# Kernel tuning notes

Hardware: AMD Instinct MI355X
Metric: run time of the kernel (lower is better)

Reference implementation:

```python
import jax, jax.numpy as jnp
import numpy as np

B = 524288
H = 20          # heads
NUM_EX = 13     # embedding rows
EMB = 3         # embedding dim
FEAT_IN, FEAT_OUT = 3, 5
HEAD_IN, HEAD_HID = 8, 10


def setup_inputs() -> dict:
    key = jax.random.key(0)
    ks = jax.random.split(key, 12)
    e = jax.random.randint(ks[0], (B, H), 0, NUM_EX)
    f = jax.random.normal(ks[1], (B, H * FEAT_IN), dtype=jnp.float32)
    # embedding table; row 0 zeroed as in the torch __init__
    emb = jax.random.normal(ks[2], (NUM_EX, EMB), dtype=jnp.float32) * 0.1
    emb = emb.at[0].set(0.0)
    # features Linear(3 -> 5), stored as (in, out) so y = x @ Wf + bf
    Wf = jax.random.normal(ks[3], (FEAT_IN, FEAT_OUT), dtype=jnp.float32) * 0.5
    bf = jax.random.normal(ks[4], (FEAT_OUT,), dtype=jnp.float32) * 0.1
    # 20 parallel head MLPs, batched over the head axis
    W1 = jax.random.normal(ks[5], (H, HEAD_IN, HEAD_HID), dtype=jnp.float32) * 0.3
    b1 = jax.random.normal(ks[6], (H, HEAD_HID), dtype=jnp.float32) * 0.1
    W2 = jax.random.normal(ks[7], (H, HEAD_HID), dtype=jnp.float32) * 0.3
    b2 = jax.random.normal(ks[8], (H,), dtype=jnp.float32) * 0.1
    # output Linear(20 -> 1)
    Wo = jax.random.normal(ks[9], (H, 1), dtype=jnp.float32) * 0.3
    bo = jax.random.normal(ks[10], (1,), dtype=jnp.float32) * 0.1
    return {"e": e, "f": f, "emb": emb, "Wf": Wf, "bf": bf,
            "W1": W1, "b1": b1, "W2": W2, "b2": b2, "Wo": Wo, "bo": bo}


def reference(e, f, emb, Wf, bf, W1, b1, W2, b2, Wo, bo):
    ev = emb[e]                                    # (B, 20, 3) embedding lookup
    fv = f.reshape(-1, H, FEAT_IN) @ Wf + bf       # (B, 20, 5)
    x = jnp.concatenate([ev, fv], axis=2)          # (B, 20, 8)
    # all 20 heads as one batched matmul instead of a Python loop
    h1 = jax.nn.leaky_relu(jnp.einsum('bhi,hio->bho', x, W1) + b1)  # (B, 20, 10)
    h = jax.nn.softplus(jnp.einsum('bho,ho->bh', h1, W2) + b2)      # (B, 20)
    return h @ Wo + bo                             # (B, 1)
```

## Files before the change

kernel.cpp:

```cpp
#include <hip/hip_runtime.h>


#define HH   20
#define NEX  13
#define TST  12
#define WS_M 0
#define WS_T 640
#define NT   512

typedef __attribute__((ext_vector_type(4))) _Float16 half4;

__device__ __forceinline__ float softplus_fast(float x) {
    return fmaxf(x, 0.0f) + __logf(1.0f + __expf(-fabsf(x)));
}

__global__ void airfit_setup(const float* __restrict__ emb,
                             const float* __restrict__ Wf,
                             const float* __restrict__ bf,
                             const float* __restrict__ W1,
                             const float* __restrict__ b1,
                             float* __restrict__ ws)
{
    int t = blockIdx.x * 256 + threadIdx.x;
    if (t < HH * 3 * 10) {
        int h = t / 30, c = (t / 10) % 3, o = t % 10;
        float a = 0.0f;
        for (int q = 0; q < 5; ++q)
            a += Wf[c * 5 + q] * W1[(h * 8 + 3 + q) * 10 + o];
        ws[WS_M + (h * 3 + c) * 10 + o] = a;
    }
    if (t < HH * NEX * 10) {
        int h = t / (NEX * 10), idx = (t / 10) % NEX, o = t % 10;
        float a = b1[h * 10 + o];
        for (int i = 0; i < 3; ++i)
            a += emb[idx * 3 + i] * W1[(h * 8 + i) * 10 + o];
        for (int q = 0; q < 5; ++q)
            a += bf[q] * W1[(h * 8 + 3 + q) * 10 + o];
        ws[WS_T + (h * NEX + idx) * TST + o] = a;
    }
}

__global__ __launch_bounds__(NT, 4) void airfit_kernel(
    const int*   __restrict__ e,   const float* __restrict__ f,
    const float* __restrict__ ws,  const float* __restrict__ W2,
    const float* __restrict__ b2,  const float* __restrict__ Wo,
    const float* __restrict__ bo,  float* __restrict__ out, int B)
{
    __shared__ half4          s_fh[15][NT];
    __shared__ unsigned short s_e[NT * 6];
    __shared__ float          s_T[HH * NEX * TST];

    const int tid  = threadIdx.x;
    const int base = blockIdx.x * NT;
    const int nIt  = min(NT, B - base);

    for (int t = tid; t < HH * NEX * TST; t += NT)
        s_T[t] = ws[WS_T + t];

    {
        const float4* fg = reinterpret_cast<const float4*>(f) + (size_t)base * 15;
        const int total4 = nIt * 15;
#pragma unroll
        for (int k = 0; k < 15; ++k) {
            int idx = tid + NT * k;
            if (idx < total4) {
                float4 v = fg[idx];
                int item = idx / 15, c4 = idx - item * 15;
                half4 hv = { (_Float16)v.x, (_Float16)v.y,
                             (_Float16)v.z, (_Float16)v.w };
                s_fh[c4][item] = hv;
            }
        }
    }

    {
        const int4* eg = reinterpret_cast<const int4*>(e) + (size_t)base * 5;
        const int total4 = nIt * 5;
#pragma unroll
        for (int k = 0; k < 5; ++k) {
            int idx = tid + NT * k;
            if (idx < total4) {
                int4 iv = eg[idx];
                int item = idx / 5, g = idx - item * 5;
                unsigned p = (unsigned)iv.x | ((unsigned)iv.y << 4) |
                             ((unsigned)iv.z << 8) | ((unsigned)iv.w << 12);
                s_e[item * 6 + g] = (unsigned short)p;
            }
        }
    }

    __syncthreads();

    if (tid >= nIt) return;
    const float* M = ws + WS_M;

    const unsigned* e32 = reinterpret_cast<const unsigned*>(s_e);
    unsigned ew[3] = { e32[tid * 3 + 0], e32[tid * 3 + 1], e32[tid * 3 + 2] };

    float acc = bo[0];

#pragma unroll
    for (int g = 0; g < 5; ++g) {
        half4 a0 = s_fh[3 * g + 0][tid];
        half4 a1 = s_fh[3 * g + 1][tid];
        half4 a2 = s_fh[3 * g + 2][tid];
        float ff[12] = { (float)a0.x, (float)a0.y, (float)a0.z, (float)a0.w,
                         (float)a1.x, (float)a1.y, (float)a1.z, (float)a1.w,
                         (float)a2.x, (float)a2.y, (float)a2.z, (float)a2.w };
        unsigned gw  = ew[g >> 1] >> ((g & 1) * 16);

#pragma unroll
        for (int t = 0; t < 4; ++t) {
            const int h = 4 * g + t;
            int idx = (gw >> (4 * t)) & 0xf;

            const float* Trow = s_T + (h * NEX + idx) * TST;
            float4 t0 = *reinterpret_cast<const float4*>(Trow);
            float4 t1 = *reinterpret_cast<const float4*>(Trow + 4);
            float2 t2 = *reinterpret_cast<const float2*>(Trow + 8);
            float pre[10] = { t0.x, t0.y, t0.z, t0.w,
                              t1.x, t1.y, t1.z, t1.w, t2.x, t2.y };

            float g0 = ff[3 * t + 0], g1 = ff[3 * t + 1], g2 = ff[3 * t + 2];
            float hacc = b2[h];
#pragma unroll
            for (int o = 0; o < 10; ++o) {
                float a = pre[o];
                a = fmaf(g0, M[(h * 3 + 0) * 10 + o], a);
                a = fmaf(g1, M[(h * 3 + 1) * 10 + o], a);
                a = fmaf(g2, M[(h * 3 + 2) * 10 + o], a);
                a = fmaxf(a, 0.01f * a);
                hacc = fmaf(a, W2[h * 10 + o], hacc);
            }
            acc = fmaf(softplus_fast(hacc), Wo[h], acc);
        }
    }

    out[base + tid] = acc;
}

extern "C" void kernel_launch(void* const* d_in, const int* in_sizes, int n_in,
                              void* d_out, int out_size, void* d_ws, size_t ws_size,
                              hipStream_t stream) {
    const int*   e   = (const int*)  d_in[0];
    const float* f   = (const float*)d_in[1];
    const float* emb = (const float*)d_in[2];
    const float* Wf  = (const float*)d_in[3];
    const float* bf  = (const float*)d_in[4];
    const float* W1  = (const float*)d_in[5];
    const float* b1  = (const float*)d_in[6];
    const float* W2  = (const float*)d_in[7];
    const float* b2  = (const float*)d_in[8];
    const float* Wo  = (const float*)d_in[9];
    const float* bo  = (const float*)d_in[10];
    float* out = (float*)d_out;
    float* ws  = (float*)d_ws;

    int B = in_sizes[0] / HH;

    airfit_setup<<<11, 256, 0, stream>>>(emb, Wf, bf, W1, b1, ws);

    int blocks = (B + NT - 1) / NT;
    airfit_kernel<<<blocks, NT, 0, stream>>>(e, f, ws, W2, b2, Wo, bo, out, B);
}
```

Baseline: 253.4 us.

## Switch head MLP to packed fp16 math and drop shared-memory input staging

Precomputed tables and weights are now stored as packed fp16 pairs. The hidden layer uses packed half FMAs plus fdot2 for the W2 reduction, which is meant to cut ALU instruction count. Inputs e and f are read directly per thread instead of being staged through LDS, which shrinks shared memory use and allows occupancy to rise to 8 blocks per CU. The trade-off is that per-thread strided global loads are less coalesced, and doing the pre-activation in fp16 lowers accuracy.

Result: slower. 279.9 us (+10.4%).

```diff
diff --git a/kernel.cpp b/kernel.cpp
--- a/kernel.cpp
+++ b/kernel.cpp
@@ -3,15 +3,25 @@
 
 #define HH   20
 #define NEX  13
-#define TST  12
-#define WS_M 0
-#define WS_T 640
 #define NT   512
 
-typedef __attribute__((ext_vector_type(4))) _Float16 half4;
+#define WS_T   0
+#define WS_M   1560
+#define WS_WB  1880
+#define WS_END 2040
+
+typedef _Float16 hv2 __attribute__((ext_vector_type(2)));
 
 __device__ __forceinline__ float softplus_fast(float x) {
     return fmaxf(x, 0.0f) + __logf(1.0f + __expf(-fabsf(x)));
+}
+
+__device__ __forceinline__ float fdot2f(hv2 a, hv2 b, float c) {
+#if __has_builtin(__builtin_amdgcn_fdot2)
+    return __builtin_amdgcn_fdot2(a, b, c, false);
+#else
+    return fmaf((float)a.x, (float)b.x, fmaf((float)a.y, (float)b.y, c));
+#endif
 }
 
 __global__ void airfit_setup(const float* __restrict__ emb,
@@ -19,124 +29,132 @@
                              const float* __restrict__ bf,
                              const float* __restrict__ W1,
                              const float* __restrict__ b1,
+                             const float* __restrict__ W2,
+                             const float* __restrict__ b2,
+                             const float* __restrict__ Wo,
                              float* __restrict__ ws)
 {
     int t = blockIdx.x * 256 + threadIdx.x;
-    if (t < HH * 3 * 10) {
-        int h = t / 30, c = (t / 10) % 3, o = t % 10;
-        float a = 0.0f;
-        for (int q = 0; q < 5; ++q)
-            a += Wf[c * 5 + q] * W1[(h * 8 + 3 + q) * 10 + o];
-        ws[WS_M + (h * 3 + c) * 10 + o] = a;
+    hv2* wsh = reinterpret_cast<hv2*>(ws);
+
+    if (t < HH * NEX * 6) {
+        int h = t / (NEX * 6), r = t % (NEX * 6), idx = r / 6, p = r % 6;
+        float v[2] = { 0.0f, 0.0f };
+        if (p < 5) {
+            for (int s = 0; s < 2; ++s) {
+                int o = 2 * p + s;
+                float a = b1[h * 10 + o];
+                for (int i = 0; i < 3; ++i)
+                    a += emb[idx * 3 + i] * W1[(h * 8 + i) * 10 + o];
+                for (int q = 0; q < 5; ++q)
+                    a += bf[q] * W1[(h * 8 + 3 + q) * 10 + o];
+                v[s] = a;
+            }
+        }
+        wsh[WS_T + t] = hv2{ (_Float16)v[0], (_Float16)v[1] };
     }
-    if (t < HH * NEX * 10) {
-        int h = t / (NEX * 10), idx = (t / 10) % NEX, o = t % 10;
-        float a = b1[h * 10 + o];
-        for (int i = 0; i < 3; ++i)
-            a += emb[idx * 3 + i] * W1[(h * 8 + i) * 10 + o];
-        for (int q = 0; q < 5; ++q)
-            a += bf[q] * W1[(h * 8 + 3 + q) * 10 + o];
-        ws[WS_T + (h * NEX + idx) * TST + o] = a;
+    if (t < HH * 16) {
+        int h = t / 16, s = t % 16;
+        float v[2] = { 0.0f, 0.0f };
+        if (s < 15) {
+            int c = s / 5, pp = s % 5;
+            for (int sd = 0; sd < 2; ++sd) {
+                int o = 2 * pp + sd;
+                float a = 0.0f;
+                for (int q = 0; q < 5; ++q)
+                    a += Wf[c * 5 + q] * W1[(h * 8 + 3 + q) * 10 + o];
+                v[sd] = a;
+            }
+        }
+        wsh[WS_M + t] = hv2{ (_Float16)v[0], (_Float16)v[1] };
+    }
+    if (t < HH * 8) {
+        int h = t / 8, s = t % 8;
+        float outv = 0.0f;
+        if (s < 5)
+            outv = __builtin_bit_cast(float,
+                       hv2{ (_Float16)W2[h * 10 + 2 * s],
+                            (_Float16)W2[h * 10 + 2 * s + 1] });
+        else if (s == 5) outv = b2[h];
+        else if (s == 6) outv = Wo[h];
+        ws[WS_WB + t] = outv;
     }
 }
 
-__global__ __launch_bounds__(NT, 4) void airfit_kernel(
+__global__ __launch_bounds__(NT, 8) void airfit_kernel(
     const int*   __restrict__ e,   const float* __restrict__ f,
-    const float* __restrict__ ws,  const float* __restrict__ W2,
-    const float* __restrict__ b2,  const float* __restrict__ Wo,
-    const float* __restrict__ bo,  float* __restrict__ out, int B)
+    const float* __restrict__ ws,  const float* __restrict__ bo,
+    float* __restrict__ out, int B)
 {
-    __shared__ half4          s_fh[15][NT];
-    __shared__ unsigned short s_e[NT * 6];
-    __shared__ float          s_T[HH * NEX * TST];
+    __shared__ __align__(16) float s_c[WS_END];
 
     const int tid  = threadIdx.x;
     const int base = blockIdx.x * NT;
     const int nIt  = min(NT, B - base);
 
-    for (int t = tid; t < HH * NEX * TST; t += NT)
-        s_T[t] = ws[WS_T + t];
-
-    {
-        const float4* fg = reinterpret_cast<const float4*>(f) + (size_t)base * 15;
-        const int total4 = nIt * 15;
-#pragma unroll
-        for (int k = 0; k < 15; ++k) {
-            int idx = tid + NT * k;
-            if (idx < total4) {
-                float4 v = fg[idx];
-                int item = idx / 15, c4 = idx - item * 15;
-                half4 hv = { (_Float16)v.x, (_Float16)v.y,
-                             (_Float16)v.z, (_Float16)v.w };
-                s_fh[c4][item] = hv;
-            }
-        }
-    }
-
-    {
-        const int4* eg = reinterpret_cast<const int4*>(e) + (size_t)base * 5;
-        const int total4 = nIt * 5;
-#pragma unroll
-        for (int k = 0; k < 5; ++k) {
-            int idx = tid + NT * k;
-            if (idx < total4) {
-                int4 iv = eg[idx];
-                int item = idx / 5, g = idx - item * 5;
-                unsigned p = (unsigned)iv.x | ((unsigned)iv.y << 4) |
-                             ((unsigned)iv.z << 8) | ((unsigned)iv.w << 12);
-                s_e[item * 6 + g] = (unsigned short)p;
-            }
-        }
-    }
-
+    for (int t = tid; t < WS_END; t += NT) s_c[t] = ws[t];
     __syncthreads();
 
     if (tid >= nIt) return;
-    const float* M = ws + WS_M;
+    const int item = base + tid;
 
-    const unsigned* e32 = reinterpret_cast<const unsigned*>(s_e);
-    unsigned ew[3] = { e32[tid * 3 + 0], e32[tid * 3 + 1], e32[tid * 3 + 2] };
+    const int4* eg = reinterpret_cast<const int4*>(e + (size_t)item * HH);
+    int4 e0 = eg[0], e1 = eg[1], e2 = eg[2], e3 = eg[3], e4 = eg[4];
+    unsigned ew0 = (unsigned)(e0.x & 15)        | ((unsigned)(e0.y & 15) << 4)
+                 | ((unsigned)(e0.z & 15) << 8) | ((unsigned)(e0.w & 15) << 12)
+                 | ((unsigned)(e1.x & 15) << 16)| ((unsigned)(e1.y & 15) << 20)
+                 | ((unsigned)(e1.z & 15) << 24)| ((unsigned)(e1.w & 15) << 28);
+    unsigned ew1 = (unsigned)(e2.x & 15)        | ((unsigned)(e2.y & 15) << 4)
+                 | ((unsigned)(e2.z & 15) << 8) | ((unsigned)(e2.w & 15) << 12)
+                 | ((unsigned)(e3.x & 15) << 16)| ((unsigned)(e3.y & 15) << 20)
+                 | ((unsigned)(e3.z & 15) << 24)| ((unsigned)(e3.w & 15) << 28);
+    unsigned ew2 = (unsigned)(e4.x & 15)        | ((unsigned)(e4.y & 15) << 4)
+                 | ((unsigned)(e4.z & 15) << 8) | ((unsigned)(e4.w & 15) << 12);
+
+    const float2* fg = reinterpret_cast<const float2*>(f) + (size_t)item * 30;
+    hv2 fh[30];
+#pragma unroll
+    for (int k = 0; k < 30; ++k) {
+        float2 v = fg[k];
+        fh[k] = hv2{ (_Float16)v.x, (_Float16)v.y };
+    }
+
+    const hv2* Tt = reinterpret_cast<const hv2*>(s_c + WS_T);
+    const hv2* Mt = reinterpret_cast<const hv2*>(s_c + WS_M);
+    const hv2 lk2 = hv2{ (_Float16)0.01f, (_Float16)0.01f };
 
     float acc = bo[0];
+#pragma unroll
+    for (int h = 0; h < HH; ++h) {
+        unsigned word = (h < 8) ? ew0 : ((h < 16) ? ew1 : ew2);
+        int idx = (int)((word >> (4 * (h & 7))) & 0xfu);
 
+        const hv2* Tr = Tt + (h * NEX + idx) * 6;
+        hv2 tp[5] = { Tr[0], Tr[1], Tr[2], Tr[3], Tr[4] };
+
+        const int kb = (3 * h) >> 1;
+        _Float16 x0, x1, x2;
+        if ((h & 1) == 0) { x0 = fh[kb].x;  x1 = fh[kb].y;  x2 = fh[kb+1].x; }
+        else              { x0 = fh[kb].y;  x1 = fh[kb+1].x; x2 = fh[kb+1].y; }
+        hv2 g0 = hv2{ x0, x0 }, g1 = hv2{ x1, x1 }, g2 = hv2{ x2, x2 };
+
+        const hv2*   Mh  = Mt + h * 16;
+        const float* wb  = s_c + WS_WB + h * 8;
+        const hv2*   W2h = reinterpret_cast<const hv2*>(wb);
+
+        float hacc = wb[5];
 #pragma unroll
-    for (int g = 0; g < 5; ++g) {
-        half4 a0 = s_fh[3 * g + 0][tid];
-        half4 a1 = s_fh[3 * g + 1][tid];
-        half4 a2 = s_fh[3 * g + 2][tid];
-        float ff[12] = { (float)a0.x, (float)a0.y, (float)a0.z, (float)a0.w,
-                         (float)a1.x, (float)a1.y, (float)a1.z, (float)a1.w,
-                         (float)a2.x, (float)a2.y, (float)a2.z, (float)a2.w };
-        unsigned gw  = ew[g >> 1] >> ((g & 1) * 16);
-
-#pragma unroll
-        for (int t = 0; t < 4; ++t) {
-            const int h = 4 * g + t;
-            int idx = (gw >> (4 * t)) & 0xf;
-
-            const float* Trow = s_T + (h * NEX + idx) * TST;
-            float4 t0 = *reinterpret_cast<const float4*>(Trow);
-            float4 t1 = *reinterpret_cast<const float4*>(Trow + 4);
-            float2 t2 = *reinterpret_cast<const float2*>(Trow + 8);
-            float pre[10] = { t0.x, t0.y, t0.z, t0.w,
-                              t1.x, t1.y, t1.z, t1.w, t2.x, t2.y };
-
-            float g0 = ff[3 * t + 0], g1 = ff[3 * t + 1], g2 = ff[3 * t + 2];
-            float hacc = b2[h];
-#pragma unroll
-            for (int o = 0; o < 10; ++o) {
-                float a = pre[o];
-                a = fmaf(g0, M[(h * 3 + 0) * 10 + o], a);
-                a = fmaf(g1, M[(h * 3 + 1) * 10 + o], a);
-                a = fmaf(g2, M[(h * 3 + 2) * 10 + o], a);
-                a = fmaxf(a, 0.01f * a);
-                hacc = fmaf(a, W2[h * 10 + o], hacc);
-            }
-            acc = fmaf(softplus_fast(hacc), Wo[h], acc);
+        for (int p = 0; p < 5; ++p) {
+            hv2 v = g0 * Mh[p] + tp[p];
+            v = g1 * Mh[5 + p] + v;
+            v = g2 * Mh[10 + p] + v;
+            v = __builtin_elementwise_max(v, v * lk2);
+            hacc = fdot2f(v, W2h[p], hacc);
         }
+        acc = fmaf(softplus_fast(hacc), wb[6], acc);
     }
 
-    out[base + tid] = acc;
+    out[item] = acc;
 }
 
 extern "C" void kernel_launch(void* const* d_in, const int* in_sizes, int n_in,
@@ -158,8 +176,9 @@
 
     int B = in_sizes[0] / HH;
 
-    airfit_setup<<<11, 256, 0, stream>>>(emb, Wf, bf, W1, b1, ws);
+    int sblocks = (HH * NEX * 6 + 255) / 256;
+    airfit_setup<<<sblocks, 256, 0, stream>>>(emb, Wf, bf, W1, b1, W2, b2, Wo, ws);
 
     int blocks = (B + NT - 1) / NT;
-    airfit_kernel<<<blocks, NT, 0, stream>>>(e, f, ws, W2, b2, Wo, bo, out, B);
+    airfit_kernel<<<blocks, NT, 0, stream>>>(e, f, ws, bo, out, B);
 }
```
